# Optimization experiments

Hardware: AMD Instinct MI355X
Metric: run time of the kernel (lower is better)

The kernel has to match this reference:

```python
import jax, jax.numpy as jnp
import numpy as np

HEADS = 8
DIM_HEAD = 64
T = 16            # temporal_length
MAX_REL = T       # max_relative_position
QUERY_DIM = 320
INNER = HEADS * DIM_HEAD
NEG = -1e9


def _sparse_causal_mask(t):
    m1 = np.tril(np.ones((t, t), dtype=bool))
    m2 = np.zeros((t, t), dtype=np.float32)
    m2[2:t, : t - 2] = np.tril(np.ones((t - 2, t - 2), dtype=np.float32))
    return m1 & (1 - m2).astype(bool)  # [t, t]


def _rel_idx(t, max_rel):
    r = np.arange(t)
    dist = np.clip(r[None, :] - r[:, None], -max_rel, max_rel) + max_rel
    return dist.astype(np.int32)  # [t, t]


def setup_inputs() -> dict:
    key = jax.random.key(0)
    ks = jax.random.split(key, 8)
    B = 8192
    s = 0.02
    return {
        "x": jax.random.normal(ks[0], (B, T, QUERY_DIM), dtype=jnp.float32),
        "Wq": jax.random.normal(ks[1], (QUERY_DIM, INNER), dtype=jnp.float32) * s,
        "Wk": jax.random.normal(ks[2], (QUERY_DIM, INNER), dtype=jnp.float32) * s,
        "Wv": jax.random.normal(ks[3], (QUERY_DIM, INNER), dtype=jnp.float32) * s,
        "Wo": jax.random.normal(ks[4], (INNER, QUERY_DIM), dtype=jnp.float32) * s,
        "bo": jnp.zeros((QUERY_DIM,), dtype=jnp.float32),
        "rel_k_table": jax.random.normal(ks[5], (2 * MAX_REL + 1, DIM_HEAD), dtype=jnp.float32) * s,
        "rel_v_table": jax.random.normal(ks[6], (2 * MAX_REL + 1, DIM_HEAD), dtype=jnp.float32) * s,
    }


def reference(x, Wq, Wk, Wv, Wo, bo, rel_k_table, rel_v_table):
    b, n, _ = x.shape
    scale = DIM_HEAD ** -0.5

    def split_heads(t):  # [b,n,inner] -> [b,h,n,d]
        return t.reshape(b, n, HEADS, DIM_HEAD).transpose(0, 2, 1, 3)

    q = split_heads(x @ Wq)
    k = split_heads(x @ Wk)
    v = split_heads(x @ Wv)

    sim = jnp.einsum("bhid,bhjd->bhij", q, k) * scale  # [b,h,n,n]

    idx = jnp.asarray(_rel_idx(n, MAX_REL))
    k2 = rel_k_table[idx]  # [n,n,d]
    sim = sim + jnp.einsum("bhtd,tsd->bhts", q, k2) * scale

    mask = jnp.asarray(_sparse_causal_mask(n))  # [n,n] bool
    sim = sim + (1.0 - mask.astype(sim.dtype)) * NEG

    attn = jax.nn.softmax(sim, axis=-1)
    out = jnp.einsum("bhij,bhjd->bhid", attn, v)

    v2 = rel_v_table[idx]  # [n,n,d]
    out = out + jnp.einsum("bhts,tsd->bhtd", attn, v2)

    out = out.transpose(0, 2, 1, 3).reshape(b, n, INNER)
    return out @ Wo + bo
```

## Files before the change

### kernel.cpp

```cpp
#include <hip/hip_runtime.h>


typedef __attribute__((ext_vector_type(8))) short short8;
typedef __attribute__((ext_vector_type(4))) float floatx4;

#define NWQKV (8*192*320)
#define NWO   (320*512)

__device__ __forceinline__ unsigned short f2b(float x) {
  union { float f; unsigned int u; } t; t.f = x;
  unsigned int r = t.u + 0x7FFFu + ((t.u >> 16) & 1u);
  return (unsigned short)(r >> 16);
}

typedef const __attribute__((address_space(1))) unsigned int* gas_ptr;
typedef __attribute__((address_space(3))) unsigned int* las_ptr;

__device__ __forceinline__ void gload16(const void* g, void* l) {
  __builtin_amdgcn_global_load_lds((gas_ptr)g, (las_ptr)l, 16, 0, 0);
}

__global__ __launch_bounds__(256) void prep_kernel(
    const float* __restrict__ Wq, const float* __restrict__ Wk,
    const float* __restrict__ Wv, const float* __restrict__ Wo,
    unsigned short* __restrict__ wqkvT, unsigned short* __restrict__ woT) {
  int tid = blockIdx.x * 256 + threadIdx.x;
  if (tid < NWQKV) {
    int k = tid % 320;
    int c = (tid / 320) % 192;
    int h = tid / (320 * 192);
    int sel = c >> 6, d = c & 63;
    const float* W = (sel == 0) ? Wq : ((sel == 1) ? Wk : Wv);
    wqkvT[tid] = f2b(W[k * 512 + h * 64 + d]);
  } else {
    int i = tid - NWQKV;
    int k = i & 511;
    int c = i >> 9;
    woT[i] = f2b(Wo[k * 320 + c]);
  }
}

__global__ __launch_bounds__(512, 2) void qkv_attn_kernel(
    const float* __restrict__ x, const float* __restrict__ relk,
    const float* __restrict__ relv, const unsigned short* __restrict__ wqkvT,
    unsigned short* __restrict__ attnout) {
  __shared__ short8 bq[2][768];
  const int tid = threadIdx.x;
  const int lane = tid & 63;
  const int w = tid >> 6;
  const int lr = lane & 15;
  const int g = lane >> 4;
  const int wr0 = blockIdx.x * 256 + w * 32;

  float rk15v[4], rk16v[4], rv15v[4], rv16v[4];
#pragma unroll
  for (int f = 0; f < 4; f++) {
    int d = f * 16 + lr;
    rk15v[f] = relk[15 * 64 + d];
    rk16v[f] = relk[16 * 64 + d];
    rv15v[f] = relv[15 * 64 + d];
    rv16v[f] = relv[16 * 64 + d];
  }

  short8 af[2][10];
#pragma unroll
  for (int r = 0; r < 2; r++) {
    const float* xrow = x + (size_t)(wr0 + r * 16 + lr) * 320;
#pragma unroll
    for (int ks = 0; ks < 10; ks++) {
      const float4 u0 = *(const float4*)(xrow + ks * 32 + g * 8);
      const float4 u1 = *(const float4*)(xrow + ks * 32 + g * 8 + 4);
      short8 a;
      a[0] = (short)f2b(u0.x); a[1] = (short)f2b(u0.y);
      a[2] = (short)f2b(u0.z); a[3] = (short)f2b(u0.w);
      a[4] = (short)f2b(u1.x); a[5] = (short)f2b(u1.y);
      a[6] = (short)f2b(u1.z); a[7] = (short)f2b(u1.w);
      af[r][ks] = a;
    }
  }

  floatx4 acc[2][12];
#pragma unroll
  for (int r = 0; r < 2; r++)
#pragma unroll
    for (int f = 0; f < 12; f++) acc[r][f] = (floatx4){0.f, 0.f, 0.f, 0.f};

  auto stage = [&](int h, int ks, int cb) {
    const unsigned short* wb = wqkvT + h * 61440 + ks * 32;
    {
      int nf = w;
      gload16(wb + (nf * 16 + lr) * 320 + g * 8, &bq[cb][nf * 64]);
    }
    if (w < 4) {
      int nf = 8 + w;
      gload16(wb + (nf * 16 + lr) * 320 + g * 8, &bq[cb][nf * 64]);
    }
  };

  stage(0, 0, 0);
  for (int h = 0; h < 8; ++h) {
#pragma unroll
    for (int ksi = 0; ksi < 10; ++ksi) {
      const int cb = ksi & 1;
      __syncthreads();
      if (h * 10 + ksi < 79) {
        int ksn = (ksi == 9) ? 0 : ksi + 1;
        int hn = (ksi == 9) ? h + 1 : h;
        stage(hn, ksn, cb ^ 1);
      }
#pragma unroll
      for (int nf = 0; nf < 12; ++nf) {
        short8 b = bq[cb][nf * 64 + lane];
        acc[0][nf] = __builtin_amdgcn_mfma_f32_16x16x32_bf16(af[0][ksi], b, acc[0][nf], 0, 0, 0);
        acc[1][nf] = __builtin_amdgcn_mfma_f32_16x16x32_bf16(af[1][ksi], b, acc[1][nf], 0, 0, 0);
      }
    }

#pragma unroll
    for (int r = 0; r < 2; ++r) {
      float s0[4], s1[4];
#pragma unroll
      for (int reg = 0; reg < 4; ++reg) {
        float c0 = 0.f, c1 = 0.f;
#pragma unroll
        for (int f = 0; f < 4; ++f) {
          float q = acc[r][f][reg];
          float kk = acc[r][4 + f][reg];
          float kp = (reg > 0) ? acc[r][4 + f][reg - 1]
                               : __shfl(acc[r][4 + f][3], (lane - 16) & 63, 64);
          c0 += q * (kk + rk16v[f]);
          c1 += q * (kp + rk15v[f]);
        }
#pragma unroll
        for (int m = 1; m < 16; m <<= 1) {
          c0 += __shfl_xor(c0, m, 16);
          c1 += __shfl_xor(c1, m, 16);
        }
        s0[reg] = c0 * 0.125f;
        s1[reg] = c1 * 0.125f;
      }
#pragma unroll
      for (int reg = 0; reg < 4; ++reg) {
        int t = g * 4 + reg;
        float S0 = s0[reg], S1 = s1[reg];
        float mm = fmaxf(S0, S1);
        float e0 = __expf(S0 - mm), e1 = __expf(S1 - mm);
        float inv = 1.f / (e0 + e1);
        float a0 = (t == 0) ? 1.f : e0 * inv;
        float a1 = (t == 0) ? 0.f : e1 * inv;
        size_t base = (size_t)(wr0 + r * 16 + t) * 512 + h * 64 + lr;
#pragma unroll
        for (int f = 0; f < 4; ++f) {
          float vv = acc[r][8 + f][reg];
          float vp = (reg > 0) ? acc[r][8 + f][reg - 1]
                               : __shfl(acc[r][8 + f][3], (lane - 16) & 63, 64);
          attnout[base + f * 16] = f2b(a0 * (vv + rv16v[f]) + a1 * (vp + rv15v[f]));
        }
      }
    }
#pragma unroll
    for (int r = 0; r < 2; ++r)
#pragma unroll
      for (int f = 0; f < 12; ++f) acc[r][f] = (floatx4){0.f, 0.f, 0.f, 0.f};
  }
}

__global__ __launch_bounds__(512, 4) void out_proj_kernel(
    const unsigned short* __restrict__ attnout,
    const unsigned short* __restrict__ woT,
    const float* __restrict__ bo, float* __restrict__ out) {
  __shared__ short8 sB[2][1280];
  __shared__ short8 sA[2][512];
  const int tid = threadIdx.x;
  const int lane = tid & 63;
  const int w = tid >> 6;
  const int lr = lane & 15;
  const int g = lane >> 4;
  const int rg = w >> 1, half = w & 1;
  const int rowbase = blockIdx.x * 128;

  auto stage = [&](int s, int cb) {
    const int ko = s * 32 + g * 8;
    { int c = w;      gload16(woT + (c * 16 + lr) * 512 + ko, &sB[cb][c * 64]); }
    { int c = 8 + w;  gload16(woT + (c * 16 + lr) * 512 + ko, &sB[cb][c * 64]); }
    if (w < 4) { int c = 16 + w;
                 gload16(woT + (c * 16 + lr) * 512 + ko, &sB[cb][c * 64]); }
    gload16(attnout + (size_t)(rowbase + w * 16 + lr) * 512 + ko, &sA[cb][w * 64]);
  };

  floatx4 acc[2][10];
#pragma unroll
  for (int r = 0; r < 2; r++)
#pragma unroll
    for (int f = 0; f < 10; f++) acc[r][f] = (floatx4){0.f, 0.f, 0.f, 0.f};

  stage(0, 0);
  for (int kt = 0; kt < 8; ++kt) {
#pragma unroll
    for (int ph = 0; ph < 2; ++ph) {
      const int cb = ph;
      const int s = kt * 2 + ph;
      __syncthreads();
      if (s < 15) stage(s + 1, cb ^ 1);
      short8 a0 = sA[cb][(rg * 2 + 0) * 64 + lane];
      short8 a1 = sA[cb][(rg * 2 + 1) * 64 + lane];
#pragma unroll
      for (int nf = 0; nf < 10; ++nf) {
        short8 b = sB[cb][(half * 10 + nf) * 64 + lane];
        acc[0][nf] = __builtin_amdgcn_mfma_f32_16x16x32_bf16(a0, b, acc[0][nf], 0, 0, 0);
        acc[1][nf] = __builtin_amdgcn_mfma_f32_16x16x32_bf16(a1, b, acc[1][nf], 0, 0, 0);
      }
    }
  }

#pragma unroll
  for (int r = 0; r < 2; ++r)
#pragma unroll
    for (int nf = 0; nf < 10; ++nf) {
      int col = half * 160 + nf * 16 + lr;
      float bb = bo[col];
#pragma unroll
      for (int reg = 0; reg < 4; ++reg) {
        int row = rowbase + rg * 32 + r * 16 + g * 4 + reg;
        out[(size_t)row * 320 + col] = acc[r][nf][reg] + bb;
      }
    }
}

extern "C" void kernel_launch(void* const* d_in, const int* in_sizes, int n_in,
                              void* d_out, int out_size, void* d_ws, size_t ws_size,
                              hipStream_t stream) {
  (void)in_sizes; (void)n_in; (void)out_size; (void)ws_size;
  const float* x    = (const float*)d_in[0];
  const float* Wq   = (const float*)d_in[1];
  const float* Wk   = (const float*)d_in[2];
  const float* Wv   = (const float*)d_in[3];
  const float* Wo   = (const float*)d_in[4];
  const float* bo   = (const float*)d_in[5];
  const float* relk = (const float*)d_in[6];
  const float* relv = (const float*)d_in[7];
  float* out = (float*)d_out;

  unsigned short* wqkvT   = (unsigned short*)d_ws;
  unsigned short* woT     = wqkvT + NWQKV;
  unsigned short* attnout = woT + NWO;

  prep_kernel<<<(NWQKV + NWO) / 256, 256, 0, stream>>>(Wq, Wk, Wv, Wo, wqkvT, woT);
  qkv_attn_kernel<<<512, 512, 0, stream>>>(x, relk, relv, wqkvT, attnout);
  out_proj_kernel<<<1024, 512, 0, stream>>>(attnout, woT, bo, out);
}
```

Measured before the change: 529.1 us.

## Retile QKV-attention into per-head Q/K then V passes; hold A in registers for out-proj

The QKV-attention kernel now uses 256-thread blocks where each wave owns three 16-row sequences. Each head is split into two pipelined passes: Q/K first to compute the two-tap softmax weights, then V. Weights are staged in 64-wide k chunks, so each barrier covers more MFMA work and B-fragment reuse rises across three row tiles. The out-projection kernel now loads its attention-output A fragments straight into registers and stages only Wo in LDS with larger k steps, cutting the number of barriers. The trade-offs are higher register pressure, a ragged last block that needs clamped loads and guarded stores, and lower occupancy limits.

```diff
diff --git a/kernel.cpp b/kernel.cpp
--- a/kernel.cpp
+++ b/kernel.cpp
@@ -6,6 +6,7 @@
 
 #define NWQKV (8*192*320)
 #define NWO   (320*512)
+#define NRS   8192
 
 __device__ __forceinline__ unsigned short f2b(float x) {
   union { float f; unsigned int u; } t; t.f = x;
@@ -40,17 +41,41 @@
   }
 }
 
-__global__ __launch_bounds__(512, 2) void qkv_attn_kernel(
+__global__ __launch_bounds__(256, 2) void qkv_attn_kernel(
     const float* __restrict__ x, const float* __restrict__ relk,
     const float* __restrict__ relv, const unsigned short* __restrict__ wqkvT,
     unsigned short* __restrict__ attnout) {
-  __shared__ short8 bq[2][768];
+  __shared__ short8 bq1[2][1024];
+  __shared__ short8 bq2[2][512];
   const int tid = threadIdx.x;
   const int lane = tid & 63;
   const int w = tid >> 6;
   const int lr = lane & 15;
   const int g = lane >> 4;
-  const int wr0 = blockIdx.x * 256 + w * 32;
+  const int rs0 = blockIdx.x * 12 + w * 3;
+
+  auto stage1 = [&](int h, int p, int cb) {
+    const unsigned short* wb = wqkvT + h * 61440;
+#pragma unroll
+    for (int i = 0; i < 4; i++) {
+      int slot = w * 4 + i;
+      int nf = slot & 7, ksub = slot >> 3;
+      gload16(wb + (nf * 16 + lr) * 320 + p * 64 + ksub * 32 + g * 8,
+              &bq1[cb][slot * 64]);
+    }
+  };
+  auto stage2 = [&](int h, int p, int cb) {
+    const unsigned short* wb = wqkvT + h * 61440 + 40960;
+#pragma unroll
+    for (int i = 0; i < 2; i++) {
+      int slot = w * 2 + i;
+      int nf = slot & 3, ksub = slot >> 2;
+      gload16(wb + (nf * 16 + lr) * 320 + p * 64 + ksub * 32 + g * 8,
+              &bq2[cb][slot * 64]);
+    }
+  };
+
+  stage1(0, 0, 0);
 
   float rk15v[4], rk16v[4], rv15v[4], rv16v[4];
 #pragma unroll
@@ -62,10 +87,11 @@
     rv16v[f] = relv[16 * 64 + d];
   }
 
-  short8 af[2][10];
-#pragma unroll
-  for (int r = 0; r < 2; r++) {
-    const float* xrow = x + (size_t)(wr0 + r * 16 + lr) * 320;
+  short8 af[3][10];
+#pragma unroll
+  for (int rs = 0; rs < 3; rs++) {
+    int rsg = rs0 + rs; if (rsg > NRS - 1) rsg = NRS - 1;
+    const float* xrow = x + (size_t)(rsg * 16 + lr) * 320;
 #pragma unroll
     for (int ks = 0; ks < 10; ks++) {
       const float4 u0 = *(const float4*)(xrow + ks * 32 + g * 8);
@@ -75,59 +101,48 @@
       a[2] = (short)f2b(u0.z); a[3] = (short)f2b(u0.w);
       a[4] = (short)f2b(u1.x); a[5] = (short)f2b(u1.y);
       a[6] = (short)f2b(u1.z); a[7] = (short)f2b(u1.w);
-      af[r][ks] = a;
-    }
-  }
-
-  floatx4 acc[2][12];
-#pragma unroll
-  for (int r = 0; r < 2; r++)
-#pragma unroll
-    for (int f = 0; f < 12; f++) acc[r][f] = (floatx4){0.f, 0.f, 0.f, 0.f};
-
-  auto stage = [&](int h, int ks, int cb) {
-    const unsigned short* wb = wqkvT + h * 61440 + ks * 32;
-    {
-      int nf = w;
-      gload16(wb + (nf * 16 + lr) * 320 + g * 8, &bq[cb][nf * 64]);
-    }
-    if (w < 4) {
-      int nf = 8 + w;
-      gload16(wb + (nf * 16 + lr) * 320 + g * 8, &bq[cb][nf * 64]);
-    }
-  };
-
-  stage(0, 0, 0);
+      af[rs][ks] = a;
+    }
+  }
+
+#pragma unroll 1
   for (int h = 0; h < 8; ++h) {
-#pragma unroll
-    for (int ksi = 0; ksi < 10; ++ksi) {
-      const int cb = ksi & 1;
+    floatx4 acc1[3][8];
+#pragma unroll
+    for (int rs = 0; rs < 3; rs++)
+#pragma unroll
+      for (int nf = 0; nf < 8; nf++) acc1[rs][nf] = (floatx4){0.f,0.f,0.f,0.f};
+
+#pragma unroll
+    for (int p = 0; p < 5; ++p) {
+      const int cb = p & 1;
       __syncthreads();
-      if (h * 10 + ksi < 79) {
-        int ksn = (ksi == 9) ? 0 : ksi + 1;
-        int hn = (ksi == 9) ? h + 1 : h;
-        stage(hn, ksn, cb ^ 1);
-      }
-#pragma unroll
-      for (int nf = 0; nf < 12; ++nf) {
-        short8 b = bq[cb][nf * 64 + lane];
-        acc[0][nf] = __builtin_amdgcn_mfma_f32_16x16x32_bf16(af[0][ksi], b, acc[0][nf], 0, 0, 0);
-        acc[1][nf] = __builtin_amdgcn_mfma_f32_16x16x32_bf16(af[1][ksi], b, acc[1][nf], 0, 0, 0);
-      }
-    }
-
-#pragma unroll
-    for (int r = 0; r < 2; ++r) {
-      float s0[4], s1[4];
-#pragma unroll
-      for (int reg = 0; reg < 4; ++reg) {
+      if (p < 4) stage1(h, p + 1, cb ^ 1);
+      else       stage2(h, 0, 0);
+#pragma unroll
+      for (int ksub = 0; ksub < 2; ++ksub)
+#pragma unroll
+        for (int nf = 0; nf < 8; ++nf) {
+          short8 b = bq1[cb][(ksub * 8 + nf) * 64 + lane];
+#pragma unroll
+          for (int rs = 0; rs < 3; rs++)
+            acc1[rs][nf] = __builtin_amdgcn_mfma_f32_16x16x32_bf16(
+                af[rs][p * 2 + ksub], b, acc1[rs][nf], 0, 0, 0);
+        }
+    }
+
+    float a0[3][4], a1[3][4];
+#pragma unroll
+    for (int rs = 0; rs < 3; rs++) {
+#pragma unroll
+      for (int reg = 0; reg < 4; reg++) {
         float c0 = 0.f, c1 = 0.f;
 #pragma unroll
-        for (int f = 0; f < 4; ++f) {
-          float q = acc[r][f][reg];
-          float kk = acc[r][4 + f][reg];
-          float kp = (reg > 0) ? acc[r][4 + f][reg - 1]
-                               : __shfl(acc[r][4 + f][3], (lane - 16) & 63, 64);
+        for (int f = 0; f < 4; f++) {
+          float q  = acc1[rs][f][reg];
+          float kk = acc1[rs][4 + f][reg];
+          float kp = (reg > 0) ? acc1[rs][4 + f][reg - 1]
+                               : __shfl(acc1[rs][4 + f][3], (lane - 16) & 63, 64);
           c0 += q * (kk + rk16v[f]);
           c1 += q * (kp + rk15v[f]);
         }
@@ -136,93 +151,127 @@
           c0 += __shfl_xor(c0, m, 16);
           c1 += __shfl_xor(c1, m, 16);
         }
-        s0[reg] = c0 * 0.125f;
-        s1[reg] = c1 * 0.125f;
-      }
-#pragma unroll
-      for (int reg = 0; reg < 4; ++reg) {
+        float S0 = c0 * 0.125f, S1 = c1 * 0.125f;
         int t = g * 4 + reg;
-        float S0 = s0[reg], S1 = s1[reg];
         float mm = fmaxf(S0, S1);
         float e0 = __expf(S0 - mm), e1 = __expf(S1 - mm);
         float inv = 1.f / (e0 + e1);
-        float a0 = (t == 0) ? 1.f : e0 * inv;
-        float a1 = (t == 0) ? 0.f : e1 * inv;
-        size_t base = (size_t)(wr0 + r * 16 + t) * 512 + h * 64 + lr;
-#pragma unroll
-        for (int f = 0; f < 4; ++f) {
-          float vv = acc[r][8 + f][reg];
-          float vp = (reg > 0) ? acc[r][8 + f][reg - 1]
-                               : __shfl(acc[r][8 + f][3], (lane - 16) & 63, 64);
-          attnout[base + f * 16] = f2b(a0 * (vv + rv16v[f]) + a1 * (vp + rv15v[f]));
-        }
+        a0[rs][reg] = (t == 0) ? 1.f : e0 * inv;
+        a1[rs][reg] = (t == 0) ? 0.f : e1 * inv;
       }
     }
-#pragma unroll
-    for (int r = 0; r < 2; ++r)
-#pragma unroll
-      for (int f = 0; f < 12; ++f) acc[r][f] = (floatx4){0.f, 0.f, 0.f, 0.f};
-  }
-}
-
-__global__ __launch_bounds__(512, 4) void out_proj_kernel(
+
+    floatx4 accv[3][4];
+#pragma unroll
+    for (int rs = 0; rs < 3; rs++)
+#pragma unroll
+      for (int nf = 0; nf < 4; nf++) accv[rs][nf] = (floatx4){0.f,0.f,0.f,0.f};
+
+#pragma unroll
+    for (int p = 0; p < 5; ++p) {
+      const int cb = p & 1;
+      __syncthreads();
+      if (p < 4)      stage2(h, p + 1, cb ^ 1);
+      else if (h < 7) stage1(h + 1, 0, 0);
+#pragma unroll
+      for (int ksub = 0; ksub < 2; ++ksub)
+#pragma unroll
+        for (int nf = 0; nf < 4; ++nf) {
+          short8 b = bq2[cb][(ksub * 4 + nf) * 64 + lane];
+#pragma unroll
+          for (int rs = 0; rs < 3; rs++)
+            accv[rs][nf] = __builtin_amdgcn_mfma_f32_16x16x32_bf16(
+                af[rs][p * 2 + ksub], b, accv[rs][nf], 0, 0, 0);
+        }
+    }
+
+#pragma unroll
+    for (int rs = 0; rs < 3; rs++) {
+      const bool valid = (rs0 + rs) < NRS;
+#pragma unroll
+      for (int reg = 0; reg < 4; reg++) {
+        int t = g * 4 + reg;
+        size_t base = (size_t)((size_t)(rs0 + rs) * 16 + t) * 512 + h * 64 + lr;
+#pragma unroll
+        for (int f = 0; f < 4; f++) {
+          float vv = accv[rs][f][reg];
+          float vp = (reg > 0) ? accv[rs][f][reg - 1]
+                               : __shfl(accv[rs][f][3], (lane - 16) & 63, 64);
+          float o = a0[rs][reg] * (vv + rv16v[f]) + a1[rs][reg] * (vp + rv15v[f]);
+          if (valid) attnout[base + f * 16] = f2b(o);
+        }
+      }
+    }
+  }
+}
+
+__global__ __launch_bounds__(512, 2) void out_proj_kernel(
     const unsigned short* __restrict__ attnout,
     const unsigned short* __restrict__ woT,
     const float* __restrict__ bo, float* __restrict__ out) {
-  __shared__ short8 sB[2][1280];
-  __shared__ short8 sA[2][512];
+  __shared__ short8 sB[2][2560];
   const int tid = threadIdx.x;
   const int lane = tid & 63;
   const int w = tid >> 6;
   const int lr = lane & 15;
   const int g = lane >> 4;
-  const int rg = w >> 1, half = w & 1;
-  const int rowbase = blockIdx.x * 128;
-
-  auto stage = [&](int s, int cb) {
-    const int ko = s * 32 + g * 8;
-    { int c = w;      gload16(woT + (c * 16 + lr) * 512 + ko, &sB[cb][c * 64]); }
-    { int c = 8 + w;  gload16(woT + (c * 16 + lr) * 512 + ko, &sB[cb][c * 64]); }
-    if (w < 4) { int c = 16 + w;
-                 gload16(woT + (c * 16 + lr) * 512 + ko, &sB[cb][c * 64]); }
-    gload16(attnout + (size_t)(rowbase + w * 16 + lr) * 512 + ko, &sA[cb][w * 64]);
+  const int mg = w >> 1, nh = w & 1;
+  const int row0 = blockIdx.x * 128 + mg * 32;
+
+  auto stage = [&](int p, int cb) {
+#pragma unroll
+    for (int i = 0; i < 5; i++) {
+      int slot = w * 5 + i;
+      int nf = slot % 20, ksub = slot / 20;
+      gload16(woT + (nf * 16 + lr) * 512 + p * 64 + ksub * 32 + g * 8,
+              &sB[cb][slot * 64]);
+    }
   };
 
+  stage(0, 0);
+
+  short8 af[2][16];
+#pragma unroll
+  for (int rs = 0; rs < 2; rs++) {
+    const unsigned short* ar = attnout + (size_t)(row0 + rs * 16 + lr) * 512;
+#pragma unroll
+    for (int ks = 0; ks < 16; ks++)
+      af[rs][ks] = *(const short8*)(ar + ks * 32 + g * 8);
+  }
+
   floatx4 acc[2][10];
 #pragma unroll
-  for (int r = 0; r < 2; r++)
-#pragma unroll
-    for (int f = 0; f < 10; f++) acc[r][f] = (floatx4){0.f, 0.f, 0.f, 0.f};
-
-  stage(0, 0);
-  for (int kt = 0; kt < 8; ++kt) {
-#pragma unroll
-    for (int ph = 0; ph < 2; ++ph) {
-      const int cb = ph;
-      const int s = kt * 2 + ph;
-      __syncthreads();
-      if (s < 15) stage(s + 1, cb ^ 1);
-      short8 a0 = sA[cb][(rg * 2 + 0) * 64 + lane];
-      short8 a1 = sA[cb][(rg * 2 + 1) * 64 + lane];
-#pragma unroll
-      for (int nf = 0; nf < 10; ++nf) {
-        short8 b = sB[cb][(half * 10 + nf) * 64 + lane];
-        acc[0][nf] = __builtin_amdgcn_mfma_f32_16x16x32_bf16(a0, b, acc[0][nf], 0, 0, 0);
-        acc[1][nf] = __builtin_amdgcn_mfma_f32_16x16x32_bf16(a1, b, acc[1][nf], 0, 0, 0);
+  for (int rs = 0; rs < 2; rs++)
+#pragma unroll
+    for (int j = 0; j < 10; j++) acc[rs][j] = (floatx4){0.f, 0.f, 0.f, 0.f};
+
+#pragma unroll
+  for (int p = 0; p < 8; ++p) {
+    const int cb = p & 1;
+    __syncthreads();
+    if (p < 7) stage(p + 1, cb ^ 1);
+#pragma unroll
+    for (int ksub = 0; ksub < 2; ++ksub)
+#pragma unroll
+      for (int j = 0; j < 10; ++j) {
+        short8 b = sB[cb][(ksub * 20 + nh * 10 + j) * 64 + lane];
+#pragma unroll
+        for (int rs = 0; rs < 2; rs++)
+          acc[rs][j] = __builtin_amdgcn_mfma_f32_16x16x32_bf16(
+              af[rs][p * 2 + ksub], b, acc[rs][j], 0, 0, 0);
       }
-    }
-  }
-
-#pragma unroll
-  for (int r = 0; r < 2; ++r)
-#pragma unroll
-    for (int nf = 0; nf < 10; ++nf) {
-      int col = half * 160 + nf * 16 + lr;
+  }
+
+#pragma unroll
+  for (int rs = 0; rs < 2; rs++)
+#pragma unroll
+    for (int j = 0; j < 10; ++j) {
+      int col = nh * 160 + j * 16 + lr;
       float bb = bo[col];
 #pragma unroll
-      for (int reg = 0; reg < 4; ++reg) {
-        int row = rowbase + rg * 32 + r * 16 + g * 4 + reg;
-        out[(size_t)row * 320 + col] = acc[r][nf][reg] + bb;
+      for (int reg = 0; reg < 4; reg++) {
+        int row = row0 + rs * 16 + g * 4 + reg;
+        out[(size_t)row * 320 + col] = acc[rs][j][reg] + bb;
       }
     }
 }
@@ -246,6 +295,6 @@
   unsigned short* attnout = woT + NWO;
 
   prep_kernel<<<(NWQKV + NWO) / 256, 256, 0, stream>>>(Wq, Wk, Wv, Wo, wqkvT, woT);
-  qkv_attn_kernel<<<512, 512, 0, stream>>>(x, relk, relv, wqkvT, attnout);
+  qkv_attn_kernel<<<683, 256, 0, stream>>>(x, relk, relv, wqkvT, attnout);
   out_proj_kernel<<<1024, 512, 0, stream>>>(attnout, woT, bo, out);
 }
```

Result: slower. 790.4 us (+49.4%).
